# Optimization experiments

Measured on AMD Instinct MI355X. Metric: run time of the kernel, lower is better.

## Reference

```python
import jax, jax.numpy as jnp
import numpy as np

N = 10000   # num_nodes (batch=1)
E = 160000  # num edges
CIN, H, T, OUT, K = 32, 64, 12, 12, 3


def _conv1d(x, w, b, pad):
    # x: [N, C_in, T], w: [C_out, C_in, K]
    out = jax.lax.conv_general_dilated(
        x, w, window_strides=(1,), padding=[(pad, pad)],
        dimension_numbers=('NCH', 'OIH', 'NCH'))
    return out + b[None, :, None]


def _gated_tconv(x, w, b):
    # GatedTemporalConv (dropout = identity in eval)
    out = _conv1d(x, w, b, K // 2)
    P, Q = jnp.split(out, 2, axis=1)
    return P * jax.nn.sigmoid(Q)


def _gcn(x, W, b, src, dst, ew):
    # PyG GCNConv, vectorized over all T timesteps in one fused pass.
    # x: [N, C_in, T], W: [C_out, C_in]
    xt = jnp.einsum('nct,oc->not', x, W)
    loop = jnp.arange(N)
    srcl = jnp.concatenate([src, loop])
    dstl = jnp.concatenate([dst, loop])
    ewl = jnp.concatenate([ew, jnp.ones((N,), ew.dtype)])
    deg = jax.ops.segment_sum(ewl, dstl, num_segments=N)
    dis = jnp.where(deg > 0, jax.lax.rsqrt(deg), 0.0)
    norm = dis[srcl] * ewl * dis[dstl]                      # [E+N]
    msg = xt[srcl] * norm[:, None, None]                    # [E+N, C_out, T]
    out = jax.ops.segment_sum(msg, dstl, num_segments=N)    # [N, C_out, T]
    return out + b[None, :, None]


def setup_inputs() -> dict:
    key = jax.random.key(0)
    ks = jax.random.split(key, 20)
    rn = lambda k, s: jax.random.normal(k, s, jnp.float32) * 0.05
    return {
        'x': jax.random.normal(ks[0], (N, CIN, T), jnp.float32),
        'edge_index': jax.random.randint(ks[1], (2, E), 0, N),
        'edge_weight': jax.random.uniform(ks[2], (E,), jnp.float32),
        'tc1a_w': rn(ks[3], (2 * H, CIN, K)), 'tc1a_b': rn(ks[4], (2 * H,)),
        'gc1_w': rn(ks[5], (H, H)),           'gc1_b': rn(ks[6], (H,)),
        'tc1b_w': rn(ks[7], (2 * H, H, K)),   'tc1b_b': rn(ks[8], (2 * H,)),
        'tc2a_w': rn(ks[9], (2 * H, H, K)),   'tc2a_b': rn(ks[10], (2 * H,)),
        'gc2_w': rn(ks[11], (H, H)),          'gc2_b': rn(ks[12], (H,)),
        'tc2b_w': rn(ks[13], (2 * H, H, K)),  'tc2b_b': rn(ks[14], (2 * H,)),
        'fin_w': rn(ks[15], (OUT, H, T)),     'fin_b': rn(ks[16], (OUT,)),
    }


def reference(x, edge_index, edge_weight,
              tc1a_w, tc1a_b, gc1_w, gc1_b, tc1b_w, tc1b_b,
              tc2a_w, tc2a_b, gc2_w, gc2_b, tc2b_w, tc2b_b,
              fin_w, fin_b):
    src, dst = edge_index[0], edge_index[1]
    h = _gated_tconv(x, tc1a_w, tc1a_b)
    h = jax.nn.relu(_gcn(h, gc1_w, gc1_b, src, dst, edge_weight))
    h = _gated_tconv(h, tc1b_w, tc1b_b)
    h = _gated_tconv(h, tc2a_w, tc2a_b)
    h = jax.nn.relu(_gcn(h, gc2_w, gc2_b, src, dst, edge_weight))
    h = _gated_tconv(h, tc2b_w, tc2b_b)
    h = _conv1d(h, fin_w, fin_b, 0)          # [N, OUT, 1] (kernel == T)
    h = h[:, :, 0]                            # squeeze(-1)
    return h.reshape(1, N, OUT)               # batch_size = 1
```

## Files before the change

kernel.cpp:

```cpp
#include <hip/hip_runtime.h>
#include <hip/hip_bf16.h>
#include <stdint.h>

#define N_NODES 10000
#define N_EDGES 160000

typedef unsigned short u16;
typedef unsigned int u32;
typedef short s16v8 __attribute__((ext_vector_type(8)));
typedef float f32v4 __attribute__((ext_vector_type(4)));

__device__ __forceinline__ float bf2f(u16 v){ return __uint_as_float(((u32)v) << 16); }
__device__ __forceinline__ u16 f2bf(float f){
    u32 u = __float_as_uint(f);
    u32 r = (u + 0x7fffu + ((u >> 16) & 1u)) >> 16;
    return (u16)r;
}

struct SmallPtrs { const void* p[14]; };

__device__ __constant__ const int g_seg_off[15] = {
    0, 12288, 12416, 16512, 16576, 41152, 41280,
    65856, 65984, 70080, 70144, 94720, 94848, 104064, 104076
};
__device__ __constant__ const int g_seg_kind[14] = {
    1, 0, 0, 0, 2, 0, 2, 0, 0, 0, 2, 0, 0, 0
};

__global__ void k_convert_init(SmallPtrs ps, u16* __restrict__ dst,
                               float* deg, int* cnt, int* cur){
    int i = blockIdx.x * blockDim.x + threadIdx.x;
    if (i < 104076){
        int seg = 0, base = 0;
#pragma unroll
        for (int s = 0; s < 14; s++){
            if (i >= g_seg_off[s]){ seg = s; base = g_seg_off[s]; }
        }
        int li = i - base;
        float v = ((const float*)ps.p[seg])[li];
        int kind = g_seg_kind[seg];
        int dsto = li;
        if (kind){
            int CIN = (kind == 1) ? 32 : 64;
            int o = li / (3 * CIN);
            int rem = li - o * (3 * CIN);
            int c = rem / 3, d = rem - c * 3;
            dsto = d * 128 * CIN + o * CIN + c;
        }
        dst[base + dsto] = f2bf(v);
    }
    if (i < N_NODES){ deg[i] = 1.0f; cnt[i] = 0; cur[i] = 0; }
}

__launch_bounds__(256, 2)
__global__ void k_gconv_count(const float* __restrict__ xin, const u16* __restrict__ wg,
                              const u16* __restrict__ bg, u16* __restrict__ out,
                              const int* __restrict__ ei, const float* __restrict__ ew,
                              float* deg, int* cnt){
    if (blockIdx.x >= 1250){
        int e = (blockIdx.x - 1250) * 256 + threadIdx.x;
        if (e < N_EDGES){
            int d = ei[N_EDGES + e];
            atomicAdd(&deg[d], ew[e]);
            atomicAdd(&cnt[d], 1);
        }
        return;
    }
    __shared__ __attribute__((aligned(16))) u16 xT[8][14][40];
    __shared__ __attribute__((aligned(16))) u16 Ho[8][12][72];
    int tid = threadIdx.x;
    int n0 = blockIdx.x * 8;

    for (int i = tid; i < 8 * 40; i += 256){
        int g = i / 40, c = i % 40;
        xT[g][0][c] = 0; xT[g][13][c] = 0;
    }
    {
        int g = tid >> 5, c = tid & 31;
        const float4* p = (const float4*)(xin + ((size_t)(n0 + g) * 32 + c) * 12);
        float4 v0 = p[0], v1 = p[1], v2 = p[2];
        xT[g][1][c] = f2bf(v0.x);  xT[g][2][c] = f2bf(v0.y);
        xT[g][3][c] = f2bf(v0.z);  xT[g][4][c] = f2bf(v0.w);
        xT[g][5][c] = f2bf(v1.x);  xT[g][6][c] = f2bf(v1.y);
        xT[g][7][c] = f2bf(v1.z);  xT[g][8][c] = f2bf(v1.w);
        xT[g][9][c] = f2bf(v2.x);  xT[g][10][c] = f2bf(v2.y);
        xT[g][11][c] = f2bf(v2.z); xT[g][12][c] = f2bf(v2.w);
    }
    int lane = tid & 63, wave = tid >> 6;
    int col = lane & 15, quad = lane >> 4;
    int o_p = wave * 16 + col, o_q = o_p + 64;

    s16v8 Bf[3][2];
#pragma unroll
    for (int pq = 0; pq < 2; pq++){
        int o = pq ? o_q : o_p;
#pragma unroll
        for (int d = 0; d < 3; d++)
            Bf[d][pq] = *(const s16v8*)(wg + d * 4096 + o * 32 + quad * 8);
    }
    __syncthreads();

    f32v4 aP[6], aQ[6];
#pragma unroll
    for (int mt = 0; mt < 6; mt++){ aP[mt] = (f32v4)0.f; aQ[mt] = (f32v4)0.f; }
#pragma unroll
    for (int mt = 0; mt < 6; mt++){
        int m = mt * 16 + col;
        int g = m / 12, t = m - 12 * g;
#pragma unroll
        for (int d = 0; d < 3; d++){
            s16v8 a = *(const s16v8*)&xT[g][t + d][quad * 8];
            aP[mt] = __builtin_amdgcn_mfma_f32_16x16x32_bf16(a, Bf[d][0], aP[mt], 0, 0, 0);
            aQ[mt] = __builtin_amdgcn_mfma_f32_16x16x32_bf16(a, Bf[d][1], aQ[mt], 0, 0, 0);
        }
    }
    float bP = bf2f(bg[o_p]), bQ = bf2f(bg[o_q]);
#pragma unroll
    for (int mt = 0; mt < 6; mt++){
#pragma unroll
        for (int r = 0; r < 4; r++){
            int m2 = mt * 16 + quad * 4 + r;
            int g = m2 / 12, t = m2 - 12 * g;
            float pv = aP[mt][r] + bP, qv = aQ[mt][r] + bQ;
            Ho[g][t][o_p] = f2bf(pv / (1.f + __expf(-qv)));
        }
    }
    __syncthreads();
    for (int i = tid; i < 768; i += 256){
        int g = i / 96, r = i % 96, t = r / 8, ch = r % 8;
        *(s16v8*)(out + (size_t)(n0 + g) * 768 + t * 64 + ch * 8) = *(const s16v8*)&Ho[g][t][ch * 8];
    }
}

__global__ void k_scan_dis(const int* __restrict__ cnt, int* __restrict__ off,
                           const float* __restrict__ deg, float* __restrict__ dis){
    __shared__ int wsum[16], woff[16];
    int t = threadIdx.x;
    int lane = t & 63, wv = t >> 6;
    int base = t * 10;
    int loc[10];
    int mysum = 0;
    if (base < N_NODES){
#pragma unroll
        for (int j = 0; j < 10; j++){ loc[j] = mysum; mysum += cnt[base + j]; }
    }
    int s = mysum;
#pragma unroll
    for (int d = 1; d < 64; d <<= 1){
        int v = __shfl_up(s, d, 64);
        if (lane >= d) s += v;
    }
    if (lane == 63) wsum[wv] = s;
    __syncthreads();
    if (t < 16){
        int v = wsum[t];
        int sc = v;
#pragma unroll
        for (int d = 1; d < 16; d <<= 1){
            int u = __shfl_up(sc, d, 16);
            if (t >= d) sc += u;
        }
        woff[t] = sc - v;
        if (t == 15) off[N_NODES] = sc;
    }
    __syncthreads();
    int tbase = woff[wv] + (s - mysum);
    if (base < N_NODES){
#pragma unroll
        for (int j = 0; j < 10; j++) off[base + j] = tbase + loc[j];
    }
    for (int i = t; i < N_NODES; i += 1024) dis[i] = rsqrtf(deg[i]);
}

__global__ void k_scatter(const int* __restrict__ ei, const float* __restrict__ ew,
                          const float* __restrict__ dis, const int* __restrict__ off,
                          int* cur, int2* __restrict__ epack){
    int e = blockIdx.x * blockDim.x + threadIdx.x;
    if (e < N_EDGES){
        int s = ei[e];
        int d = ei[N_EDGES + e];
        float nw = dis[s] * ew[e] * dis[d];
        int p = off[d] + atomicAdd(&cur[d], 1);
        epack[p] = make_int2(s, __float_as_int(nw));
    }
}

#define XIDX(g, row, c) (((g) * 14 + (row)) * 72 + (c))

template<bool LAST>
__launch_bounds__(256, 6)
__global__ void k_fused(const u16* __restrict__ src,
                        const float* __restrict__ dis, const int* __restrict__ off,
                        const int2* __restrict__ ep,
                        const u16* __restrict__ Wmix, const u16* __restrict__ bmix,
                        const u16* __restrict__ w1, const u16* __restrict__ b1,
                        const u16* __restrict__ w2, const u16* __restrict__ b2,
                        const u16* __restrict__ fw, const u16* __restrict__ fb,
                        u16* __restrict__ outMid, float* __restrict__ outFin){
    __shared__ __attribute__((aligned(16))) u16 bufX[4 * 14 * 72];
    __shared__ __attribute__((aligned(16))) u16 bufY[4 * 14 * 72];
    int tid = threadIdx.x;
    int n0 = blockIdx.x * 4;
    int lane = tid & 63, wave = tid >> 6;
    int col = lane & 15, quad = lane >> 4;

    for (int i = tid; i < 4 * 72; i += 256){
        int g = i / 72, c = i % 72;
        bufX[XIDX(g, 0, c)] = 0; bufX[XIDX(g, 13, c)] = 0;
        bufY[XIDX(g, 0, c)] = 0; bufY[XIDX(g, 13, c)] = 0;
    }

    {
        int g = wave, j = lane;
        int n = n0 + g;
        float dv = dis[n];
        float sw = dv * dv;
        int j4 = j * 4;
        const u16* xr = src + (size_t)n * 768 + j4;
        float acc[12];
#pragma unroll
        for (int i = 0; i < 3; i++){
            ushort4 v = *(const ushort4*)(xr + i * 256);
            acc[i * 4 + 0] = sw * bf2f(v.x);
            acc[i * 4 + 1] = sw * bf2f(v.y);
            acc[i * 4 + 2] = sw * bf2f(v.z);
            acc[i * 4 + 3] = sw * bf2f(v.w);
        }
        int b = off[n], e = off[n + 1];
        int p = b;
        for (; p + 1 < e; p += 2){
            int2 e0 = ep[p], e1 = ep[p + 1];
            float w0 = __int_as_float(e0.y), w1v = __int_as_float(e1.y);
            const u16* q0 = src + (size_t)e0.x * 768 + j4;
            const u16* q1 = src + (size_t)e1.x * 768 + j4;
            ushort4 a0 = *(const ushort4*)(q0);
            ushort4 a1 = *(const ushort4*)(q0 + 256);
            ushort4 a2 = *(const ushort4*)(q0 + 512);
            ushort4 c0 = *(const ushort4*)(q1);
            ushort4 c1 = *(const ushort4*)(q1 + 256);
            ushort4 c2 = *(const ushort4*)(q1 + 512);
            acc[0] = fmaf(w0, bf2f(a0.x), acc[0]); acc[1] = fmaf(w0, bf2f(a0.y), acc[1]);
            acc[2] = fmaf(w0, bf2f(a0.z), acc[2]); acc[3] = fmaf(w0, bf2f(a0.w), acc[3]);
            acc[4] = fmaf(w0, bf2f(a1.x), acc[4]); acc[5] = fmaf(w0, bf2f(a1.y), acc[5]);
            acc[6] = fmaf(w0, bf2f(a1.z), acc[6]); acc[7] = fmaf(w0, bf2f(a1.w), acc[7]);
            acc[8] = fmaf(w0, bf2f(a2.x), acc[8]); acc[9] = fmaf(w0, bf2f(a2.y), acc[9]);
            acc[10] = fmaf(w0, bf2f(a2.z), acc[10]); acc[11] = fmaf(w0, bf2f(a2.w), acc[11]);
            acc[0] = fmaf(w1v, bf2f(c0.x), acc[0]); acc[1] = fmaf(w1v, bf2f(c0.y), acc[1]);
            acc[2] = fmaf(w1v, bf2f(c0.z), acc[2]); acc[3] = fmaf(w1v, bf2f(c0.w), acc[3]);
            acc[4] = fmaf(w1v, bf2f(c1.x), acc[4]); acc[5] = fmaf(w1v, bf2f(c1.y), acc[5]);
            acc[6] = fmaf(w1v, bf2f(c1.z), acc[6]); acc[7] = fmaf(w1v, bf2f(c1.w), acc[7]);
            acc[8] = fmaf(w1v, bf2f(c2.x), acc[8]); acc[9] = fmaf(w1v, bf2f(c2.y), acc[9]);
            acc[10] = fmaf(w1v, bf2f(c2.z), acc[10]); acc[11] = fmaf(w1v, bf2f(c2.w), acc[11]);
        }
        if (p < e){
            int2 e0 = ep[p];
            float w0 = __int_as_float(e0.y);
            const u16* q0 = src + (size_t)e0.x * 768 + j4;
#pragma unroll
            for (int i = 0; i < 3; i++){
                ushort4 v = *(const ushort4*)(q0 + i * 256);
                acc[i * 4 + 0] = fmaf(w0, bf2f(v.x), acc[i * 4 + 0]);
                acc[i * 4 + 1] = fmaf(w0, bf2f(v.y), acc[i * 4 + 1]);
                acc[i * 4 + 2] = fmaf(w0, bf2f(v.z), acc[i * 4 + 2]);
                acc[i * 4 + 3] = fmaf(w0, bf2f(v.w), acc[i * 4 + 3]);
            }
        }
        int t0 = j >> 4, c = j4 & 63;
#pragma unroll
        for (int i = 0; i < 3; i++){
            int t = t0 + i * 4;
            ushort4 hv;
            hv.x = f2bf(acc[i * 4 + 0]); hv.y = f2bf(acc[i * 4 + 1]);
            hv.z = f2bf(acc[i * 4 + 2]); hv.w = f2bf(acc[i * 4 + 3]);
            *(ushort4*)&bufX[XIDX(g, 1 + t, c)] = hv;
        }
    }

    int o_mix = wave * 16 + col;
    s16v8 Bm[2];
#pragma unroll
    for (int ks = 0; ks < 2; ks++)
        Bm[ks] = *(const s16v8*)(Wmix + (size_t)o_mix * 64 + ks * 32 + quad * 8);
    __syncthreads();

    {
        f32v4 accm[3];
#pragma unroll
        for (int mt = 0; mt < 3; mt++) accm[mt] = (f32v4)0.f;
#pragma unroll
        for (int mt = 0; mt < 3; mt++){
            int m = mt * 16 + col;
            int g = m / 12, t = m - 12 * g;
#pragma unroll
            for (int ks = 0; ks < 2; ks++){
                s16v8 a = *(const s16v8*)&bufX[XIDX(g, 1 + t, ks * 32 + quad * 8)];
                accm[mt] = __builtin_amdgcn_mfma_f32_16x16x32_bf16(a, Bm[ks], accm[mt], 0, 0, 0);
            }
        }
        float bm = bf2f(bmix[o_mix]);
#pragma unroll
        for (int mt = 0; mt < 3; mt++){
#pragma unroll
            for (int r = 0; r < 4; r++){
                int m2 = mt * 16 + quad * 4 + r;
                int g = m2 / 12, t = m2 - 12 * g;
                bufY[XIDX(g, 1 + t, o_mix)] = f2bf(fmaxf(accm[mt][r] + bm, 0.f));
            }
        }
    }
    __syncthreads();

    {
        int o_p = wave * 16 + col, o_q = o_p + 64;
        s16v8 Bf[3][2][2];
#pragma unroll
        for (int pq = 0; pq < 2; pq++){
            int o = pq ? o_q : o_p;
#pragma unroll
            for (int d = 0; d < 3; d++)
#pragma unroll
                for (int ks = 0; ks < 2; ks++)
                    Bf[d][ks][pq] = *(const s16v8*)(w1 + d * 8192 + o * 64 + ks * 32 + quad * 8);
        }
        f32v4 aP[3], aQ[3];
#pragma unroll
        for (int mt = 0; mt < 3; mt++){ aP[mt] = (f32v4)0.f; aQ[mt] = (f32v4)0.f; }
#pragma unroll
        for (int mt = 0; mt < 3; mt++){
            int m = mt * 16 + col;
            int g = m / 12, t = m - 12 * g;
#pragma unroll
            for (int d = 0; d < 3; d++)
#pragma unroll
                for (int ks = 0; ks < 2; ks++){
                    s16v8 a = *(const s16v8*)&bufY[XIDX(g, t + d, ks * 32 + quad * 8)];
                    aP[mt] = __builtin_amdgcn_mfma_f32_16x16x32_bf16(a, Bf[d][ks][0], aP[mt], 0, 0, 0);
                    aQ[mt] = __builtin_amdgcn_mfma_f32_16x16x32_bf16(a, Bf[d][ks][1], aQ[mt], 0, 0, 0);
                }
        }
        float bP = bf2f(b1[o_p]), bQ = bf2f(b1[o_q]);
#pragma unroll
        for (int mt = 0; mt < 3; mt++){
#pragma unroll
            for (int r = 0; r < 4; r++){
                int m2 = mt * 16 + quad * 4 + r;
                int g = m2 / 12, t = m2 - 12 * g;
                float pv = aP[mt][r] + bP, qv = aQ[mt][r] + bQ;
                u16 hv = f2bf(pv / (1.f + __expf(-qv)));
                if (LAST) bufX[g * 1008 + o_p * 12 + t] = hv;
                else      bufX[XIDX(g, 1 + t, o_p)] = hv;
            }
        }
    }
    __syncthreads();

    if (!LAST){
        int o_p = wave * 16 + col, o_q = o_p + 64;
        s16v8 Bf[3][2][2];
#pragma unroll
        for (int pq = 0; pq < 2; pq++){
            int o = pq ? o_q : o_p;
#pragma unroll
            for (int d = 0; d < 3; d++)
#pragma unroll
                for (int ks = 0; ks < 2; ks++)
                    Bf[d][ks][pq] = *(const s16v8*)(w2 + d * 8192 + o * 64 + ks * 32 + quad * 8);
        }
        f32v4 aP[3], aQ[3];
#pragma unroll
        for (int mt = 0; mt < 3; mt++){ aP[mt] = (f32v4)0.f; aQ[mt] = (f32v4)0.f; }
#pragma unroll
        for (int mt = 0; mt < 3; mt++){
            int m = mt * 16 + col;
            int g = m / 12, t = m - 12 * g;
#pragma unroll
            for (int d = 0; d < 3; d++)
#pragma unroll
                for (int ks = 0; ks < 2; ks++){
                    s16v8 a = *(const s16v8*)&bufX[XIDX(g, t + d, ks * 32 + quad * 8)];
                    aP[mt] = __builtin_amdgcn_mfma_f32_16x16x32_bf16(a, Bf[d][ks][0], aP[mt], 0, 0, 0);
                    aQ[mt] = __builtin_amdgcn_mfma_f32_16x16x32_bf16(a, Bf[d][ks][1], aQ[mt], 0, 0, 0);
                }
        }
        float bP = bf2f(b2[o_p]), bQ = bf2f(b2[o_q]);
#pragma unroll
        for (int mt = 0; mt < 3; mt++){
#pragma unroll
            for (int r = 0; r < 4; r++){
                int m2 = mt * 16 + quad * 4 + r;
                int g = m2 / 12, t = m2 - 12 * g;
                float pv = aP[mt][r] + bP, qv = aQ[mt][r] + bQ;
                bufY[XIDX(g, 1 + t, o_p)] = f2bf(pv / (1.f + __expf(-qv)));
            }
        }
        __syncthreads();
        for (int i = tid; i < 384; i += 256){
            int g = i / 96, r = i % 96, t = r / 8, ch = r % 8;
            *(s16v8*)(outMid + (size_t)(n0 + g) * 768 + t * 64 + ch * 8) =
                *(const s16v8*)&bufY[XIDX(g, 1 + t, ch * 8)];
        }
    } else {
        if (wave == 0){
            f32v4 accF = {0.f, 0.f, 0.f, 0.f};
            int g4 = col & 3;
#pragma unroll
            for (int ks = 0; ks < 24; ks++){
                s16v8 a = *(const s16v8*)&bufX[g4 * 1008 + ks * 32 + quad * 8];
                s16v8 bfr = {0, 0, 0, 0, 0, 0, 0, 0};
                if (col < 12)
                    bfr = *(const s16v8*)(fw + (size_t)col * 768 + ks * 32 + quad * 8);
                accF = __builtin_amdgcn_mfma_f32_16x16x32_bf16(a, bfr, accF, 0, 0, 0);
            }
            if (col < 12 && quad == 0){
                float bb = bf2f(fb[col]);
#pragma unroll
                for (int r = 0; r < 4; r++){
                    int g = r;
                    outFin[(size_t)(n0 + g) * 12 + col] = accF[r] + bb;
                }
            }
        }
    }
}

static inline size_t align256(size_t x){ return (x + 255) & ~(size_t)255; }

extern "C" void kernel_launch(void* const* d_in, const int* in_sizes, int n_in,
                              void* d_out, int out_size, void* d_ws, size_t ws_size,
                              hipStream_t stream){
    const float* x  = (const float*)d_in[0];
    const int* ei   = (const int*)d_in[1];
    const float* ew = (const float*)d_in[2];

    char* w = (char*)d_ws;
    u16* bufA    = (u16*)w;  w += align256((size_t)N_NODES * 768 * sizeof(u16));
    u16* bufB    = (u16*)w;  w += align256((size_t)N_NODES * 768 * sizeof(u16));
    float* deg   = (float*)w; w += align256(N_NODES * sizeof(float));
    float* dis   = (float*)w; w += align256(N_NODES * sizeof(float));
    int* cnt     = (int*)w;   w += align256(N_NODES * sizeof(int));
    int* off     = (int*)w;   w += align256((N_NODES + 1) * sizeof(int));
    int* cur     = (int*)w;   w += align256(N_NODES * sizeof(int));
    int2* epack  = (int2*)w;  w += align256((size_t)N_EDGES * sizeof(int2));
    u16* cvt     = (u16*)w;   w += align256(104076 * sizeof(u16));

    u16* tc1a_w = cvt + 0;
    u16* tc1a_b = cvt + 12288;
    u16* gc1_w  = cvt + 12416;
    u16* gc1_b  = cvt + 16512;
    u16* tc1b_w = cvt + 16576;
    u16* tc1b_b = cvt + 41152;
    u16* tc2a_w = cvt + 41280;
    u16* tc2a_b = cvt + 65856;
    u16* gc2_w  = cvt + 65984;
    u16* gc2_b  = cvt + 70080;
    u16* tc2b_w = cvt + 70144;
    u16* tc2b_b = cvt + 94720;
    u16* fin_w  = cvt + 94848;
    u16* fin_b  = cvt + 104064;

    SmallPtrs ps;
    ps.p[0]  = d_in[3];  ps.p[1]  = d_in[4];
    ps.p[2]  = d_in[5];  ps.p[3]  = d_in[6];
    ps.p[4]  = d_in[7];  ps.p[5]  = d_in[8];
    ps.p[6]  = d_in[9];  ps.p[7]  = d_in[10];
    ps.p[8]  = d_in[11]; ps.p[9]  = d_in[12];
    ps.p[10] = d_in[13]; ps.p[11] = d_in[14];
    ps.p[12] = d_in[15]; ps.p[13] = d_in[16];

    k_convert_init<<<(104076 + 255) / 256, 256, 0, stream>>>(ps, cvt, deg, cnt, cur);
    k_gconv_count<<<1250 + 625, 256, 0, stream>>>(x, tc1a_w, tc1a_b, bufA, ei, ew, deg, cnt);
    k_scan_dis<<<1, 1024, 0, stream>>>(cnt, off, deg, dis);
    k_scatter<<<625, 256, 0, stream>>>(ei, ew, dis, off, cur, epack);

    k_fused<false><<<2500, 256, 0, stream>>>(bufA, dis, off, epack,
                                             gc1_w, gc1_b, tc1b_w, tc1b_b,
                                             tc2a_w, tc2a_b, nullptr, nullptr,
                                             bufB, nullptr);
    k_fused<true><<<2500, 256, 0, stream>>>(bufB, dis, off, epack,
                                            gc2_w, gc2_b, tc2b_w, tc2b_b,
                                            nullptr, nullptr, fin_w, fin_b,
                                            nullptr, (float*)d_out);
}
```

Before: 254.6 us.

## Split edge gather out of fused GCN kernel into sliced gather kernel

Moves the neighbor aggregation out of the fused MFMA kernel into a separate k_gather kernel. That kernel splits each node's 768 features into 8 slices handled by separate blocks, with 8 threads per node-slice, and writes the aggregated rows to a new workspace buffer. The fused kernel now just loads these precomputed rows into shared memory, and its launch bounds rise to 8 blocks per SM. The intent is better gather parallelism and a lighter fused kernel, at the cost of an extra round trip of a 15 MB intermediate through global memory and two more launches.

```diff
diff --git a/kernel.cpp b/kernel.cpp
--- a/kernel.cpp
+++ b/kernel.cpp
@@ -185,13 +185,81 @@
     }
 }
 
+__launch_bounds__(256, 8)
+__global__ void k_gather(const u16* __restrict__ src, const float* __restrict__ dis,
+                         const int* __restrict__ off, const int2* __restrict__ ep,
+                         u16* __restrict__ z){
+    int slice = blockIdx.x & 7;
+    int nb = blockIdx.x >> 3;
+    int nl = threadIdx.x >> 3;
+    int l8 = threadIdx.x & 7;
+    int n = nb * 32 + nl;
+    if (n >= N_NODES) return;
+    int base = slice * 96 + l8 * 12;
+    const u16* xr = src + (size_t)n * 768 + base;
+    float dv = dis[n];
+    float sw = dv * dv;
+    float acc[12];
+#pragma unroll
+    for (int k = 0; k < 3; k++){
+        ushort4 v = *(const ushort4*)(xr + k * 4);
+        acc[k * 4 + 0] = sw * bf2f(v.x); acc[k * 4 + 1] = sw * bf2f(v.y);
+        acc[k * 4 + 2] = sw * bf2f(v.z); acc[k * 4 + 3] = sw * bf2f(v.w);
+    }
+    int b = off[n], e = off[n + 1];
+    int p = b;
+    for (; p + 1 < e; p += 2){
+        int2 e0 = ep[p], e1 = ep[p + 1];
+        float w0 = __int_as_float(e0.y), w1 = __int_as_float(e1.y);
+        const u16* q0 = src + (size_t)e0.x * 768 + base;
+        const u16* q1 = src + (size_t)e1.x * 768 + base;
+        ushort4 a0 = *(const ushort4*)(q0);
+        ushort4 a1 = *(const ushort4*)(q0 + 4);
+        ushort4 a2 = *(const ushort4*)(q0 + 8);
+        ushort4 c0 = *(const ushort4*)(q1);
+        ushort4 c1 = *(const ushort4*)(q1 + 4);
+        ushort4 c2 = *(const ushort4*)(q1 + 8);
+        acc[0] = fmaf(w0, bf2f(a0.x), acc[0]); acc[1] = fmaf(w0, bf2f(a0.y), acc[1]);
+        acc[2] = fmaf(w0, bf2f(a0.z), acc[2]); acc[3] = fmaf(w0, bf2f(a0.w), acc[3]);
+        acc[4] = fmaf(w0, bf2f(a1.x), acc[4]); acc[5] = fmaf(w0, bf2f(a1.y), acc[5]);
+        acc[6] = fmaf(w0, bf2f(a1.z), acc[6]); acc[7] = fmaf(w0, bf2f(a1.w), acc[7]);
+        acc[8] = fmaf(w0, bf2f(a2.x), acc[8]); acc[9] = fmaf(w0, bf2f(a2.y), acc[9]);
+        acc[10] = fmaf(w0, bf2f(a2.z), acc[10]); acc[11] = fmaf(w0, bf2f(a2.w), acc[11]);
+        acc[0] = fmaf(w1, bf2f(c0.x), acc[0]); acc[1] = fmaf(w1, bf2f(c0.y), acc[1]);
+        acc[2] = fmaf(w1, bf2f(c0.z), acc[2]); acc[3] = fmaf(w1, bf2f(c0.w), acc[3]);
+        acc[4] = fmaf(w1, bf2f(c1.x), acc[4]); acc[5] = fmaf(w1, bf2f(c1.y), acc[5]);
+        acc[6] = fmaf(w1, bf2f(c1.z), acc[6]); acc[7] = fmaf(w1, bf2f(c1.w), acc[7]);
+        acc[8] = fmaf(w1, bf2f(c2.x), acc[8]); acc[9] = fmaf(w1, bf2f(c2.y), acc[9]);
+        acc[10] = fmaf(w1, bf2f(c2.z), acc[10]); acc[11] = fmaf(w1, bf2f(c2.w), acc[11]);
+    }
+    if (p < e){
+        int2 e0 = ep[p];
+        float w0 = __int_as_float(e0.y);
+        const u16* q0 = src + (size_t)e0.x * 768 + base;
+#pragma unroll
+        for (int k = 0; k < 3; k++){
+            ushort4 v = *(const ushort4*)(q0 + k * 4);
+            acc[k * 4 + 0] = fmaf(w0, bf2f(v.x), acc[k * 4 + 0]);
+            acc[k * 4 + 1] = fmaf(w0, bf2f(v.y), acc[k * 4 + 1]);
+            acc[k * 4 + 2] = fmaf(w0, bf2f(v.z), acc[k * 4 + 2]);
+            acc[k * 4 + 3] = fmaf(w0, bf2f(v.w), acc[k * 4 + 3]);
+        }
+    }
+    u16* zo = z + (size_t)n * 768 + base;
+#pragma unroll
+    for (int k = 0; k < 3; k++){
+        ushort4 hv;
+        hv.x = f2bf(acc[k * 4 + 0]); hv.y = f2bf(acc[k * 4 + 1]);
+        hv.z = f2bf(acc[k * 4 + 2]); hv.w = f2bf(acc[k * 4 + 3]);
+        *(ushort4*)(zo + k * 4) = hv;
+    }
+}
+
 #define XIDX(g, row, c) (((g) * 14 + (row)) * 72 + (c))
 
 template<bool LAST>
-__launch_bounds__(256, 6)
-__global__ void k_fused(const u16* __restrict__ src,
-                        const float* __restrict__ dis, const int* __restrict__ off,
-                        const int2* __restrict__ ep,
+__launch_bounds__(256, 8)
+__global__ void k_fused(const u16* __restrict__ z,
                         const u16* __restrict__ Wmix, const u16* __restrict__ bmix,
                         const u16* __restrict__ w1, const u16* __restrict__ b1,
                         const u16* __restrict__ w2, const u16* __restrict__ b2,
@@ -209,73 +277,11 @@
         bufX[XIDX(g, 0, c)] = 0; bufX[XIDX(g, 13, c)] = 0;
         bufY[XIDX(g, 0, c)] = 0; bufY[XIDX(g, 13, c)] = 0;
     }
-
-    {
-        int g = wave, j = lane;
-        int n = n0 + g;
-        float dv = dis[n];
-        float sw = dv * dv;
-        int j4 = j * 4;
-        const u16* xr = src + (size_t)n * 768 + j4;
-        float acc[12];
-#pragma unroll
-        for (int i = 0; i < 3; i++){
-            ushort4 v = *(const ushort4*)(xr + i * 256);
-            acc[i * 4 + 0] = sw * bf2f(v.x);
-            acc[i * 4 + 1] = sw * bf2f(v.y);
-            acc[i * 4 + 2] = sw * bf2f(v.z);
-            acc[i * 4 + 3] = sw * bf2f(v.w);
-        }
-        int b = off[n], e = off[n + 1];
-        int p = b;
-        for (; p + 1 < e; p += 2){
-            int2 e0 = ep[p], e1 = ep[p + 1];
-            float w0 = __int_as_float(e0.y), w1v = __int_as_float(e1.y);
-            const u16* q0 = src + (size_t)e0.x * 768 + j4;
-            const u16* q1 = src + (size_t)e1.x * 768 + j4;
-            ushort4 a0 = *(const ushort4*)(q0);
-            ushort4 a1 = *(const ushort4*)(q0 + 256);
-            ushort4 a2 = *(const ushort4*)(q0 + 512);
-            ushort4 c0 = *(const ushort4*)(q1);
-            ushort4 c1 = *(const ushort4*)(q1 + 256);
-            ushort4 c2 = *(const ushort4*)(q1 + 512);
-            acc[0] = fmaf(w0, bf2f(a0.x), acc[0]); acc[1] = fmaf(w0, bf2f(a0.y), acc[1]);
-            acc[2] = fmaf(w0, bf2f(a0.z), acc[2]); acc[3] = fmaf(w0, bf2f(a0.w), acc[3]);
-            acc[4] = fmaf(w0, bf2f(a1.x), acc[4]); acc[5] = fmaf(w0, bf2f(a1.y), acc[5]);
-            acc[6] = fmaf(w0, bf2f(a1.z), acc[6]); acc[7] = fmaf(w0, bf2f(a1.w), acc[7]);
-            acc[8] = fmaf(w0, bf2f(a2.x), acc[8]); acc[9] = fmaf(w0, bf2f(a2.y), acc[9]);
-            acc[10] = fmaf(w0, bf2f(a2.z), acc[10]); acc[11] = fmaf(w0, bf2f(a2.w), acc[11]);
-            acc[0] = fmaf(w1v, bf2f(c0.x), acc[0]); acc[1] = fmaf(w1v, bf2f(c0.y), acc[1]);
-            acc[2] = fmaf(w1v, bf2f(c0.z), acc[2]); acc[3] = fmaf(w1v, bf2f(c0.w), acc[3]);
-            acc[4] = fmaf(w1v, bf2f(c1.x), acc[4]); acc[5] = fmaf(w1v, bf2f(c1.y), acc[5]);
-            acc[6] = fmaf(w1v, bf2f(c1.z), acc[6]); acc[7] = fmaf(w1v, bf2f(c1.w), acc[7]);
-            acc[8] = fmaf(w1v, bf2f(c2.x), acc[8]); acc[9] = fmaf(w1v, bf2f(c2.y), acc[9]);
-            acc[10] = fmaf(w1v, bf2f(c2.z), acc[10]); acc[11] = fmaf(w1v, bf2f(c2.w), acc[11]);
-        }
-        if (p < e){
-            int2 e0 = ep[p];
-            float w0 = __int_as_float(e0.y);
-            const u16* q0 = src + (size_t)e0.x * 768 + j4;
-#pragma unroll
-            for (int i = 0; i < 3; i++){
-                ushort4 v = *(const ushort4*)(q0 + i * 256);
-                acc[i * 4 + 0] = fmaf(w0, bf2f(v.x), acc[i * 4 + 0]);
-                acc[i * 4 + 1] = fmaf(w0, bf2f(v.y), acc[i * 4 + 1]);
-                acc[i * 4 + 2] = fmaf(w0, bf2f(v.z), acc[i * 4 + 2]);
-                acc[i * 4 + 3] = fmaf(w0, bf2f(v.w), acc[i * 4 + 3]);
-            }
-        }
-        int t0 = j >> 4, c = j4 & 63;
-#pragma unroll
-        for (int i = 0; i < 3; i++){
-            int t = t0 + i * 4;
-            ushort4 hv;
-            hv.x = f2bf(acc[i * 4 + 0]); hv.y = f2bf(acc[i * 4 + 1]);
-            hv.z = f2bf(acc[i * 4 + 2]); hv.w = f2bf(acc[i * 4 + 3]);
-            *(ushort4*)&bufX[XIDX(g, 1 + t, c)] = hv;
-        }
-    }
-
+    for (int i = tid; i < 384; i += 256){
+        int g = i / 96, r = i % 96, t = r >> 3, ch = r & 7;
+        *(s16v8*)&bufX[XIDX(g, 1 + t, ch * 8)] =
+            *(const s16v8*)(z + (size_t)(n0 + g) * 768 + t * 64 + ch * 8);
+    }
     int o_mix = wave * 16 + col;
     s16v8 Bm[2];
 #pragma unroll
@@ -415,8 +421,7 @@
                 float bb = bf2f(fb[col]);
 #pragma unroll
                 for (int r = 0; r < 4; r++){
-                    int g = r;
-                    outFin[(size_t)(n0 + g) * 12 + col] = accF[r] + bb;
+                    outFin[(size_t)(n0 + r) * 12 + col] = accF[r] + bb;
                 }
             }
         }
@@ -435,6 +440,8 @@
     char* w = (char*)d_ws;
     u16* bufA    = (u16*)w;  w += align256((size_t)N_NODES * 768 * sizeof(u16));
     u16* bufB    = (u16*)w;  w += align256((size_t)N_NODES * 768 * sizeof(u16));
+    u16* zA      = (u16*)w;  w += align256((size_t)N_NODES * 768 * sizeof(u16));
+    u16* zB      = (u16*)w;  w += align256((size_t)N_NODES * 768 * sizeof(u16));
     float* deg   = (float*)w; w += align256(N_NODES * sizeof(float));
     float* dis   = (float*)w; w += align256(N_NODES * sizeof(float));
     int* cnt     = (int*)w;   w += align256(N_NODES * sizeof(int));
@@ -472,12 +479,12 @@
     k_scan_dis<<<1, 1024, 0, stream>>>(cnt, off, deg, dis);
     k_scatter<<<625, 256, 0, stream>>>(ei, ew, dis, off, cur, epack);
 
-    k_fused<false><<<2500, 256, 0, stream>>>(bufA, dis, off, epack,
-                                             gc1_w, gc1_b, tc1b_w, tc1b_b,
+    k_gather<<<313 * 8, 256, 0, stream>>>(bufA, dis, off, epack, zA);
+    k_fused<false><<<2500, 256, 0, stream>>>(zA, gc1_w, gc1_b, tc1b_w, tc1b_b,
                                              tc2a_w, tc2a_b, nullptr, nullptr,
                                              bufB, nullptr);
-    k_fused<true><<<2500, 256, 0, stream>>>(bufB, dis, off, epack,
-                                            gc2_w, gc2_b, tc2b_w, tc2b_b,
+    k_gather<<<313 * 8, 256, 0, stream>>>(bufB, dis, off, epack, zB);
+    k_fused<true><<<2500, 256, 0, stream>>>(zB, gc2_w, gc2_b, tc2b_w, tc2b_b,
                                             nullptr, nullptr, fin_w, fin_b,
                                             nullptr, (float*)d_out);
 }
```

New measurement: 266.8 us. 1.05x slower.
